# Optimization experiments

Hardware: AMD Instinct MI355X
Metric: run time of the kernel (lower is better)

Reference implementation:

```python
import jax, jax.numpy as jnp
import numpy as np

NEG_SLOPE = 0.2


def gat_layer(x, adj, W, a_src, a_dst):
    # x: (C, in_dim), adj: (C, C) 0/1, W: (in_dim, H*D), a_src/a_dst: (H, D)
    C = x.shape[0]
    H, D = a_src.shape
    h = (x @ W).reshape(C, H, D)            # (C, H, D)
    hh = jnp.transpose(h, (1, 0, 2))        # (H, C, D)
    asrc = jnp.einsum('hcd,hd->hc', hh, a_src)  # (H, C)
    adst = jnp.einsum('hcd,hd->hc', hh, a_dst)  # (H, C)
    e = asrc[:, :, None] + adst[:, None, :]     # (H, C, C)
    e = jax.nn.leaky_relu(e, NEG_SLOPE)
    e = jnp.where(adj[None, :, :] == 0, -jnp.inf, e)
    attn = jax.nn.softmax(e, axis=-1)           # (H, C, C)
    out = jnp.einsum('hij,hjd->hid', attn, hh)  # (H, C, D)
    return jnp.transpose(out, (1, 0, 2)).reshape(C, H * D)


def setup_inputs() -> dict:
    key = jax.random.key(0)
    ks = jax.random.split(key, 12)
    B, doc_dim = 1024, 768
    C, label_dim = 4096, 768
    hidden, H = 512, 4
    D = hidden // H  # 128

    doc_x = jax.random.normal(ks[0], (B, doc_dim), dtype=jnp.float32)
    label_init = jax.random.normal(ks[1], (C, label_dim), dtype=jnp.float32)
    adj = jax.random.randint(ks[2], (C, C), 0, 2, dtype=jnp.int32)
    adj = adj.at[jnp.arange(C), jnp.arange(C)].set(1)  # self-loops

    def xavier(k, shape):
        fan_in, fan_out = shape[0], shape[1]
        lim = jnp.sqrt(6.0 / (fan_in + fan_out)).astype(jnp.float32)
        return jax.random.uniform(k, shape, jnp.float32, -lim, lim)

    W1 = xavier(ks[3], (label_dim, hidden))
    a_src1 = xavier(ks[4], (H, D))
    a_dst1 = xavier(ks[5], (H, D))
    W2 = xavier(ks[6], (hidden, hidden))
    a_src2 = xavier(ks[7], (H, D))
    a_dst2 = xavier(ks[8], (H, D))
    Wd = xavier(ks[9], (doc_dim, hidden))
    bd = jnp.zeros((hidden,), jnp.float32)
    return {"doc_x": doc_x, "label_init": label_init, "adj": adj,
            "W1": W1, "a_src1": a_src1, "a_dst1": a_dst1,
            "W2": W2, "a_src2": a_src2, "a_dst2": a_dst2,
            "Wd": Wd, "bd": bd}


def reference(doc_x, label_init, adj, W1, a_src1, a_dst1, W2, a_src2, a_dst2, Wd, bd):
    # doc_proj (dropout = identity in eval)
    doc_h = jax.nn.relu(doc_x @ Wd + bd)            # (B, hidden)
    # label encoder: GAT -> ELU -> GAT
    h = gat_layer(label_init, adj, W1, a_src1, a_dst1)
    h = jax.nn.elu(h)
    label_h = gat_layer(h, adj, W2, a_src2, a_dst2)  # (C, hidden)
    logits = doc_h @ label_h.T                      # (B, C)
    return logits
```

## Files before the change

kernel.cpp:

```cpp
#include <hip/hip_runtime.h>
#include <hip/hip_bf16.h>
#include <math.h>

#define BDOCS   1024
#define CNODES  4096
#define INDIM   768
#define HID     512
#define NHEAD   4
#define HDIM    128
#define NEG_SLOPE 0.2f

#define KSPLIT  8
#define JPER    (CNODES / KSPLIT)
#define NCH     (JPER / 32)

typedef __attribute__((ext_vector_type(8))) short short8;
typedef __attribute__((ext_vector_type(4))) float f32x4;

__device__ __forceinline__ float lrelu(float x) { return x > 0.f ? x : NEG_SLOPE * x; }

__device__ __forceinline__ short f2bf(float f) {
    union { float f; unsigned u; } v; v.f = f;
    unsigned r = (v.u + 0x7fff + ((v.u >> 16) & 1)) >> 16;
    return (short)r;
}
__device__ __forceinline__ float bf2f(short s) {
    union { float f; unsigned u; } v; v.u = ((unsigned)(unsigned short)s) << 16;
    return v.f;
}
__device__ __forceinline__ unsigned pk2(float a, float b) {
    union { float f; unsigned u; } x, y; x.f = a; y.f = b;
    unsigned lo = (x.u + 0x7fff + ((x.u >> 16) & 1)) >> 16;
    unsigned hi = (y.u + 0x7fff + ((y.u >> 16) & 1)) >> 16;
    return lo | (hi << 16);
}
__device__ __forceinline__ short hup(float f) {
    union { float f; unsigned u; } v; v.f = f;
    return (short)((v.u + 0x8000) >> 16);
}

__device__ void frag_T_dev(const float* __restrict__ src, short* __restrict__ dst,
                           int N, int K, int jc, int nq, float (*tile)[132])
{
    const int t  = threadIdx.x;
    const int KC = K >> 5;
#pragma unroll
    for (int it = 0; it < 16; it++) {
        const int e = it * 256 + t;
        const int j = e >> 7, n = e & 127;
        tile[j][n] = src[(size_t)(jc * 32 + j) * N + nq * 128 + n];
    }
    __syncthreads();
#pragma unroll
    for (int s = 0; s < 2; s++) {
        const int item = s * 256 + t;
        const int nbl = item >> 6, lane = item & 63;
        const int nr = lane & 15, kq = lane >> 4;
        short8 v;
#pragma unroll
        for (int jr = 0; jr < 8; jr++)
            v[jr] = f2bf(tile[kq * 8 + jr][nbl * 16 + nr]);
        *(short8*)&dst[((size_t)((nq * 8 + nbl) * KC + jc) * 64 + lane) * 8] = v;
    }
}

__device__ void frag_A_dev(const float* __restrict__ src, short* __restrict__ dst,
                           int C, int rb, int cq, float (*tile)[132])
{
    const int t  = threadIdx.x;
    const int KC = C >> 5;
#pragma unroll
    for (int it = 0; it < 8; it++) {
        const int e = it * 256 + t;
        const int r = e >> 7, c = e & 127;
        tile[r][c] = src[(size_t)(rb * 16 + r) * C + cq * 128 + c];
    }
    __syncthreads();
    const int kcl = t >> 6, lane = t & 63;
    const int m = lane & 15, kq = lane >> 4;
    short8 v8;
#pragma unroll
    for (int j = 0; j < 8; j++) v8[j] = f2bf(tile[m][kcl * 32 + kq * 8 + j]);
    *(short8*)&dst[((size_t)(rb * KC + cq * 4 + kcl) * 64 + lane) * 8] = v8;
}

#define PREP_BLOCKS (65536 + 96 + 96 + 64 + 384 + 1536)
__global__ __launch_bounds__(256)
void prep_all(const int* __restrict__ adj, unsigned long long* __restrict__ adjb64,
              const float* __restrict__ Wd, short* __restrict__ Wdf,
              const float* __restrict__ W1, short* __restrict__ W1f,
              const float* __restrict__ W2, short* __restrict__ W2f,
              const float* __restrict__ doc_x, short* __restrict__ dxf,
              const float* __restrict__ label_init, short* __restrict__ lif)
{
    __shared__ float tile[32][132];
    int b = blockIdx.x;
    if (b < 65536) {
        const int t    = threadIdx.x;
        const int gw   = b * 4 + (t >> 6);
        const int lane = t & 63;
        const int i  = gw >> 6;
        const int j0 = (gw & 63) * 64;
        const int a  = adj[(size_t)i * CNODES + j0 + lane];
        const unsigned long long msk = __ballot(a != 0);
        if (lane == 0) adjb64[(size_t)i * 64 + (j0 >> 6)] = msk;
        return;
    }
    b -= 65536;
    if (b < 96)  { frag_T_dev(Wd, Wdf, HID, INDIM, b % 24, b / 24, tile); return; }
    b -= 96;
    if (b < 96)  { frag_T_dev(W1, W1f, HID, INDIM, b % 24, b / 24, tile); return; }
    b -= 96;
    if (b < 64)  { frag_T_dev(W2, W2f, HID, HID, b % 16, b / 16, tile); return; }
    b -= 64;
    if (b < 384) { frag_A_dev(doc_x, dxf, INDIM, b % 64, b / 64, tile); return; }
    b -= 384;
    frag_A_dev(label_init, lif, INDIM, b % 256, b / 256, tile);
}

template <int KC>
__global__ __launch_bounds__(64)
void gemm_hpre(const short* __restrict__ Af, const short* __restrict__ Bf,
               const float* __restrict__ a_src, const float* __restrict__ a_dst,
               short* __restrict__ hbTf, float* __restrict__ asrc, float* __restrict__ adst)
{
    __shared__ __align__(16) short tileT[128][24];
    const int lane = threadIdx.x;
    const int mb   = blockIdx.x;
    const int nq   = blockIdx.y;
    const int i0   = mb * 16;

    f32x4 acc[8];
#pragma unroll
    for (int c = 0; c < 8; c++) acc[c] = (f32x4){0.f, 0.f, 0.f, 0.f};

    const short* ap = Af + (size_t)mb * KC * 512 + lane * 8;
    const short* bp = Bf + (size_t)(nq * 8) * KC * 512 + lane * 8;

#pragma unroll 2
    for (int kc = 0; kc < KC; kc++) {
        short8 a = *(const short8*)(ap + (size_t)kc * 512);
#pragma unroll
        for (int c = 0; c < 8; c++) {
            short8 bf = *(const short8*)(bp + ((size_t)c * KC + kc) * 512);
            acc[c] = __builtin_amdgcn_mfma_f32_16x16x32_bf16(a, bf, acc[c], 0, 0, 0);
        }
    }

    const int col = lane & 15, q4 = lane >> 4;

#pragma unroll
    for (int c = 0; c < 8; c++) {
        uint2 u;
        u.x = pk2(acc[c][0], acc[c][1]);
        u.y = pk2(acc[c][2], acc[c][3]);
        *(uint2*)&tileT[c * 16 + col][q4 * 4] = u;
    }
    __syncthreads();
    {
        const int jc = mb >> 1, khalf = mb & 1;
        const int nr = lane & 15, kq = lane >> 4;
        if ((kq >> 1) == khalf) {
#pragma unroll
            for (int nbl = 0; nbl < 8; nbl++) {
                short8 v = *(const short8*)&tileT[nbl * 16 + nr][(kq & 1) * 8];
                *(short8*)&hbTf[(((size_t)(nq * 8 + nbl) * (CNODES / 32) + jc) * 64 + lane) * 8] = v;
            }
        }
    }

    float ssrc[4] = {}, sdst[4] = {};
#pragma unroll
    for (int c = 0; c < 8; c++) {
        const float vs = a_src[nq * 128 + c * 16 + col];
        const float vd = a_dst[nq * 128 + c * 16 + col];
#pragma unroll
        for (int r = 0; r < 4; r++) {
            ssrc[r] += acc[c][r] * vs;
            sdst[r] += acc[c][r] * vd;
        }
    }
#pragma unroll
    for (int mask = 1; mask <= 8; mask <<= 1)
#pragma unroll
        for (int r = 0; r < 4; r++) {
            ssrc[r] += __shfl_xor(ssrc[r], mask);
            sdst[r] += __shfl_xor(sdst[r], mask);
        }
    if (col == 0) {
#pragma unroll
        for (int r = 0; r < 4; r++) {
            const int row = i0 + q4 * 4 + r;
            asrc[nq * CNODES + row] = ssrc[r];
            adst[nq * CNODES + row] = sdst[r];
        }
    }
}

template <int KC>
__global__ __launch_bounds__(64)
void gemm_doc(const short* __restrict__ Af, const short* __restrict__ Bf,
              const float* __restrict__ bias, short* __restrict__ dhf)
{
    __shared__ __align__(16) short tile[16][64];
    const int lane = threadIdx.x;
    const int mb = blockIdx.x;
    const int ng = blockIdx.y;

    f32x4 acc[4];
#pragma unroll
    for (int c = 0; c < 4; c++) acc[c] = (f32x4){0.f, 0.f, 0.f, 0.f};

    const short* ap = Af + (size_t)mb * KC * 512 + lane * 8;
    const short* bp = Bf + (size_t)(ng * 4) * KC * 512 + lane * 8;

#pragma unroll 2
    for (int kc = 0; kc < KC; kc++) {
        short8 a = *(const short8*)(ap + (size_t)kc * 512);
#pragma unroll
        for (int c = 0; c < 4; c++) {
            short8 bf = *(const short8*)(bp + ((size_t)c * KC + kc) * 512);
            acc[c] = __builtin_amdgcn_mfma_f32_16x16x32_bf16(a, bf, acc[c], 0, 0, 0);
        }
    }

    const int col = lane & 15, q4 = lane >> 4;
#pragma unroll
    for (int c = 0; c < 4; c++)
#pragma unroll
        for (int r = 0; r < 4; r++) {
            float v = fmaxf(acc[c][r] + bias[ng * 64 + c * 16 + col], 0.f);
            tile[q4 * 4 + r][c * 16 + col] = f2bf(v);
        }
    __syncthreads();
    const int m = lane & 15, kq = lane >> 4;
#pragma unroll
    for (int kcl = 0; kcl < 2; kcl++) {
        short8 v = *(const short8*)&tile[m][kcl * 32 + kq * 8];
        *(short8*)&dhf[(((size_t)mb * 16 + ng * 2 + kcl) * 64 + lane) * 8] = v;
    }
}

template <int KC>
__global__ __launch_bounds__(64)
void gemm_frag(const short* __restrict__ Af, const short* __restrict__ Bf,
               float* __restrict__ Cmat, int N)
{
    const int lane = threadIdx.x;
    const int mb0  = blockIdx.x * 2;
    const int nq   = blockIdx.y;

    f32x4 acc[2][8];
#pragma unroll
    for (int f = 0; f < 2; f++)
#pragma unroll
        for (int c = 0; c < 8; c++) acc[f][c] = (f32x4){0.f, 0.f, 0.f, 0.f};

    const short* ap0 = Af + (size_t)mb0 * KC * 512 + lane * 8;
    const short* ap1 = ap0 + (size_t)KC * 512;
    const short* bp  = Bf + (size_t)(nq * 8) * KC * 512 + lane * 8;

#pragma unroll 2
    for (int kc = 0; kc < KC; kc++) {
        short8 a0 = *(const short8*)(ap0 + (size_t)kc * 512);
        short8 a1 = *(const short8*)(ap1 + (size_t)kc * 512);
#pragma unroll
        for (int c = 0; c < 8; c++) {
            short8 bf = *(const short8*)(bp + ((size_t)c * KC + kc) * 512);
            acc[0][c] = __builtin_amdgcn_mfma_f32_16x16x32_bf16(a0, bf, acc[0][c], 0, 0, 0);
            acc[1][c] = __builtin_amdgcn_mfma_f32_16x16x32_bf16(a1, bf, acc[1][c], 0, 0, 0);
        }
    }

    const int col = lane & 15, q4 = lane >> 4;
#pragma unroll
    for (int f = 0; f < 2; f++)
#pragma unroll
        for (int c = 0; c < 8; c++)
#pragma unroll
            for (int r = 0; r < 4; r++) {
                const int row = (mb0 + f) * 16 + q4 * 4 + r;
                Cmat[(size_t)row * N + nq * 128 + c * 16 + col] = acc[f][c][r];
            }
}

__global__ __launch_bounds__(1024)
void stats_exp(const float* __restrict__ adst, float* __restrict__ Mh,
               float* __restrict__ E1, float* __restrict__ E2)
{
    __shared__ float red[1024];
    __shared__ float s_mh;
    const int h = blockIdx.x, t = threadIdx.x;
    const float4 d4 = *(const float4*)(adst + (size_t)h * CNODES + t * 4);
    float m = fmaxf(fmaxf(d4.x, d4.y), fmaxf(d4.z, d4.w));
    red[t] = m; __syncthreads();
    for (int s = 512; s >= 1; s >>= 1) {
        if (t < s) red[t] = fmaxf(red[t], red[t + s]);
        __syncthreads();
    }
    if (t == 0) { s_mh = red[0]; Mh[h] = red[0]; }
    __syncthreads();
    const float mh = s_mh;
    float4 e1, e2;
    e1.x = __expf(d4.x - mh); e2.x = __expf(0.2f * (d4.x - mh));
    e1.y = __expf(d4.y - mh); e2.y = __expf(0.2f * (d4.y - mh));
    e1.z = __expf(d4.z - mh); e2.z = __expf(0.2f * (d4.z - mh));
    e1.w = __expf(d4.w - mh); e2.w = __expf(0.2f * (d4.w - mh));
    *(float4*)(E1 + (size_t)h * CNODES + t * 4) = e1;
    *(float4*)(E2 + (size_t)h * CNODES + t * 4) = e2;
}

__global__ __launch_bounds__(256, 2)
void attn_pv(const short* __restrict__ hbTf,
             const unsigned int* __restrict__ adjb,
             const float* __restrict__ asrc,
             const float* __restrict__ E1, const float* __restrict__ E2,
             const float* __restrict__ Mh,
             short* __restrict__ part, float* __restrict__ lpart)
{
    __shared__ __align__(16) short tileO[32][520];
    const int t    = threadIdx.x;
    const int w    = t >> 6;
    const int lane = t & 63;
    const int m    = lane & 15;
    const int kq   = lane >> 4;
    const int i0   = blockIdx.x * 64;
    const int ks   = blockIdx.y;
    const int js   = ks * JPER;

    const float mh = Mh[w];
    float A1[4], A2[4], T0[4];
#pragma unroll
    for (int g = 0; g < 4; g++) {
        const float as = asrc[w * CNODES + i0 + g * 16 + m];
        const float mr = lrelu(as + mh);
        A1[g] = __expf(as + mh - mr);
        A2[g] = __expf(0.2f * (as + mh) - mr);
        T0[g] = __expf(-as - mh);
    }

    f32x4 acc[4][8], accO[4];
#pragma unroll
    for (int g = 0; g < 4; g++) {
        accO[g] = (f32x4){0.f, 0.f, 0.f, 0.f};
#pragma unroll
        for (int c = 0; c < 8; c++) acc[g][c] = (f32x4){0.f, 0.f, 0.f, 0.f};
    }
    short8 ones;
#pragma unroll
    for (int q = 0; q < 8; q++) ones[q] = (short)0x3F80;

    for (int ch4 = 0; ch4 < 4; ch4++) {
        uint4 am[4];
#pragma unroll
        for (int g = 0; g < 4; g++)
            am[g] = *(const uint4*)(adjb + (size_t)(i0 + g * 16 + m) * 128 + ks * NCH + ch4 * 4);

#pragma unroll
        for (int chi = 0; chi < 4; chi++) {
            const int j0 = js + (ch4 * 4 + chi) * 32;
            unsigned aw[4];
#pragma unroll
            for (int g = 0; g < 4; g++)
                aw[g] = ((const unsigned*)&am[g])[chi] >> (kq * 8);

            const float4* p1 = (const float4*)(E1 + (size_t)w * CNODES + j0 + kq * 8);
            const float4* p2 = (const float4*)(E2 + (size_t)w * CNODES + j0 + kq * 8);
            const float4 x0 = p1[0], x1 = p1[1];
            const float4 y0 = p2[0], y1 = p2[1];
            const float e1v[8] = {x0.x, x0.y, x0.z, x0.w, x1.x, x1.y, x1.z, x1.w};
            const float e2v[8] = {y0.x, y0.y, y0.z, y0.w, y1.x, y1.y, y1.z, y1.w};

            short8 a[4];
#pragma unroll
            for (int q = 0; q < 8; q++) {
                const float e1 = e1v[q], e2 = e2v[q];
#pragma unroll
                for (int g = 0; g < 4; g++) {
                    const bool c0 = e1 > T0[g];
                    float wv = (c0 ? A1[g] : A2[g]) * (c0 ? e1 : e2);
                    wv = ((aw[g] >> q) & 1u) ? wv : 0.f;
                    a[g][q] = hup(wv);
                }
            }

            const short* bbase = hbTf + (((size_t)(w * 8) * 128 + (j0 >> 5)) * 64 + lane) * 8;
#pragma unroll
            for (int c = 0; c < 8; c++) {
                short8 bf = *(const short8*)(bbase + (size_t)c * 128 * 64 * 8);
                acc[0][c] = __builtin_amdgcn_mfma_f32_16x16x32_bf16(a[0], bf, acc[0][c], 0, 0, 0);
                acc[1][c] = __builtin_amdgcn_mfma_f32_16x16x32_bf16(a[1], bf, acc[1][c], 0, 0, 0);
                acc[2][c] = __builtin_amdgcn_mfma_f32_16x16x32_bf16(a[2], bf, acc[2][c], 0, 0, 0);
                acc[3][c] = __builtin_amdgcn_mfma_f32_16x16x32_bf16(a[3], bf, acc[3][c], 0, 0, 0);
            }
#pragma unroll
            for (int g = 0; g < 4; g++)
                accO[g] = __builtin_amdgcn_mfma_f32_16x16x32_bf16(a[g], ones, accO[g], 0, 0, 0);
        }
    }

    const int col = m, q4 = kq;
    if (m == 0) {
#pragma unroll
        for (int g = 0; g < 4; g++)
#pragma unroll
            for (int r = 0; r < 4; r++)
                lpart[((size_t)ks * NHEAD + w) * CNODES + i0 + g * 16 + q4 * 4 + r] = accO[g][r];
    }

    short* pS = part + (size_t)ks * CNODES * HID;
    for (int half = 0; half < 2; half++) {
        __syncthreads();
#pragma unroll
        for (int f = 0; f < 2; f++)
#pragma unroll
            for (int c = 0; c < 8; c++)
#pragma unroll
                for (int r = 0; r < 4; r++)
                    tileO[f * 16 + q4 * 4 + r][w * 128 + c * 16 + col] = f2bf(acc[half * 2 + f][c][r]);
        __syncthreads();
#pragma unroll
        for (int it = 0; it < 8; it++) {
            const int u   = it * 256 + t;
            const int row = u >> 6, un = u & 63;
            uint4 v = *(const uint4*)&tileO[row][un * 8];
            *(uint4*)&pS[(size_t)(i0 + half * 32 + row) * HID + un * 8] = v;
        }
    }
}

template <bool ELU>
__global__ __launch_bounds__(256)
void reduce_norm_frag(const short* __restrict__ part, const float* __restrict__ lpart,
                      short* __restrict__ dst)
{
    const int t = threadIdx.x;
    const int W = blockIdx.x * 4 + (t >> 6);
    const int lane = t & 63;
    const int rb = W >> 4, kc = W & 15;
    const int m = lane & 15, kq = lane >> 4;
    const int i = rb * 16 + m;
    const int n0 = kc * 32 + kq * 8;
    const int h = kc >> 2;

    float v[8] = {};
    float l = 0.f;
#pragma unroll
    for (int s = 0; s < KSPLIT; s++) {
        const uint4 raw = *(const uint4*)&part[(size_t)s * CNODES * HID + (size_t)i * HID + n0];
        const unsigned rr[4] = {raw.x, raw.y, raw.z, raw.w};
#pragma unroll
        for (int q = 0; q < 4; q++) {
            v[q * 2]     += bf2f((short)(rr[q] & 0xffff));
            v[q * 2 + 1] += bf2f((short)(rr[q] >> 16));
        }
        l += lpart[((size_t)s * NHEAD + h) * CNODES + i];
    }
    const float inv = 1.0f / l;
    short8 o;
#pragma unroll
    for (int q = 0; q < 8; q++) {
        float x = v[q] * inv;
        if (ELU) x = x > 0.f ? x : (__expf(x) - 1.f);
        o[q] = f2bf(x);
    }
    *(short8*)&dst[((size_t)(rb * 16 + kc) * 64 + lane) * 8] = o;
}

extern "C" void kernel_launch(void* const* d_in, const int* in_sizes, int n_in,
                              void* d_out, int out_size, void* d_ws, size_t ws_size,
                              hipStream_t stream)
{
    const float* doc_x      = (const float*)d_in[0];
    const float* label_init = (const float*)d_in[1];
    const int*   adj        = (const int*)d_in[2];
    const float* W1         = (const float*)d_in[3];
    const float* a_src1     = (const float*)d_in[4];
    const float* a_dst1     = (const float*)d_in[5];
    const float* W2         = (const float*)d_in[6];
    const float* a_src2     = (const float*)d_in[7];
    const float* a_dst2     = (const float*)d_in[8];
    const float* Wd         = (const float*)d_in[9];
    const float* bd         = (const float*)d_in[10];
    float*       out        = (float*)d_out;

    char* wsb = (char*)d_ws;
    size_t off = 0;
    auto alloc = [&](size_t bytes) -> char* {
        char* p = wsb + off;
        off = (off + bytes + 255) & ~(size_t)255;
        return p;
    };

    float* asrc  = (float*)alloc(NHEAD * CNODES * 4);
    float* adst  = (float*)alloc(NHEAD * CNODES * 4);
    float* Mh    = (float*)alloc(256);
    float* E1    = (float*)alloc(NHEAD * CNODES * 4);
    float* E2    = (float*)alloc(NHEAD * CNODES * 4);
    float* lpart = (float*)alloc((size_t)KSPLIT * NHEAD * CNODES * 4);
    unsigned int* adjb = (unsigned int*)alloc((size_t)CNODES * 128 * 4);
    short* hbTf  = (short*)alloc((size_t)CNODES * HID * 2);
    short* Wdf   = (short*)alloc((size_t)INDIM * HID * 2);
    short* W1f   = (short*)alloc((size_t)INDIM * HID * 2);
    short* W2f   = (short*)alloc((size_t)HID * HID * 2);
    short* dxf   = (short*)alloc((size_t)BDOCS * INDIM * 2);
    short* Af_li = (short*)alloc((size_t)CNODES * INDIM * 2);
    short* Af2   = (short*)alloc((size_t)CNODES * HID * 2);
    short* lhf   = (short*)alloc((size_t)CNODES * HID * 2);
    short* dhf   = (short*)alloc((size_t)BDOCS * HID * 2);
    short* part  = (short*)alloc((size_t)KSPLIT * CNODES * HID * 2);
    (void)ws_size;

    const dim3 blk(256);

    prep_all<<<PREP_BLOCKS, blk, 0, stream>>>(adj, (unsigned long long*)adjb,
                                              Wd, Wdf, W1, W1f, W2, W2f,
                                              doc_x, dxf, label_init, Af_li);

    gemm_doc<INDIM / 32><<<dim3(BDOCS / 16, HID / 64), 64, 0, stream>>>(dxf, Wdf, bd, dhf);

    gemm_hpre<INDIM / 32><<<dim3(CNODES / 16, NHEAD), 64, 0, stream>>>(
        Af_li, W1f, a_src1, a_dst1, hbTf, asrc, adst);

    stats_exp<<<NHEAD, 1024, 0, stream>>>(adst, Mh, E1, E2);
    attn_pv<<<dim3(CNODES / 64, KSPLIT), blk, 0, stream>>>(hbTf, adjb, asrc, E1, E2, Mh, part, lpart);
    reduce_norm_frag<true><<<CNODES * HID / 256 / 8, blk, 0, stream>>>(part, lpart, Af2);

    gemm_hpre<HID / 32><<<dim3(CNODES / 16, NHEAD), 64, 0, stream>>>(
        Af2, W2f, a_src2, a_dst2, hbTf, asrc, adst);

    stats_exp<<<NHEAD, 1024, 0, stream>>>(adst, Mh, E1, E2);
    attn_pv<<<dim3(CNODES / 64, KSPLIT), blk, 0, stream>>>(hbTf, adjb, asrc, E1, E2, Mh, part, lpart);
    reduce_norm_frag<false><<<CNODES * HID / 256 / 8, blk, 0, stream>>>(part, lpart, lhf);

    gemm_frag<HID / 32><<<dim3(BDOCS / 32, CNODES / 128), 64, 0, stream>>>(dhf, lhf, out, CNODES);
}
```

Measured before the change: 400.5 us.

## Fuse per-head max into GEMM via atomics and compute exp tables in attention LDS

Removes the separate stats_exp kernel. The per-head max of adst is now folded into gemm_hpre through an order-preserving float encoding and atomicMax, and each attn_pv block computes its own E1/E2 exp slices into shared memory. attn_pv is restructured to 512 threads, with each wave handling 32 rows instead of 64, which roughly halves per-thread accumulator registers and lets more waves run. In exchange, each column block recomputes its exp slice, atomics are added, and the encoded max buffer must be zeroed in prep_all.

```diff
diff --git a/kernel.cpp b/kernel.cpp
--- a/kernel.cpp
+++ b/kernel.cpp
@@ -38,6 +38,15 @@
     union { float f; unsigned u; } v; v.f = f;
     return (short)((v.u + 0x8000) >> 16);
 }
+__device__ __forceinline__ unsigned encf(float x) {
+    union { float f; unsigned u; } v; v.f = x;
+    return (v.u & 0x80000000u) ? ~v.u : (v.u | 0x80000000u);
+}
+__device__ __forceinline__ float decf(unsigned u) {
+    union { float f; unsigned u; } v;
+    v.u = (u & 0x80000000u) ? (u ^ 0x80000000u) : ~u;
+    return v.f;
+}
 
 __device__ void frag_T_dev(const float* __restrict__ src, short* __restrict__ dst,
                            int N, int K, int jc, int nq, float (*tile)[132])
@@ -91,11 +100,13 @@
               const float* __restrict__ W1, short* __restrict__ W1f,
               const float* __restrict__ W2, short* __restrict__ W2f,
               const float* __restrict__ doc_x, short* __restrict__ dxf,
-              const float* __restrict__ label_init, short* __restrict__ lif)
+              const float* __restrict__ label_init, short* __restrict__ lif,
+              unsigned* __restrict__ MhEnc)
 {
     __shared__ float tile[32][132];
     int b = blockIdx.x;
     if (b < 65536) {
+        if (b == 0 && threadIdx.x < 8) MhEnc[threadIdx.x] = 0u;
         const int t    = threadIdx.x;
         const int gw   = b * 4 + (t >> 6);
         const int lane = t & 63;
@@ -122,7 +133,8 @@
 __global__ __launch_bounds__(64)
 void gemm_hpre(const short* __restrict__ Af, const short* __restrict__ Bf,
                const float* __restrict__ a_src, const float* __restrict__ a_dst,
-               short* __restrict__ hbTf, float* __restrict__ asrc, float* __restrict__ adst)
+               short* __restrict__ hbTf, float* __restrict__ asrc, float* __restrict__ adst,
+               unsigned* __restrict__ MhEnc)
 {
     __shared__ __align__(16) short tileT[128][24];
     const int lane = threadIdx.x;
@@ -195,6 +207,10 @@
             adst[nq * CNODES + row] = sdst[r];
         }
     }
+    float wmax = fmaxf(fmaxf(sdst[0], sdst[1]), fmaxf(sdst[2], sdst[3]));
+    wmax = fmaxf(wmax, __shfl_xor(wmax, 16));
+    wmax = fmaxf(wmax, __shfl_xor(wmax, 32));
+    if (lane == 0) atomicMax(MhEnc + nq, encf(wmax));
 }
 
 template <int KC>
@@ -284,144 +300,123 @@
             }
 }
 
-__global__ __launch_bounds__(1024)
-void stats_exp(const float* __restrict__ adst, float* __restrict__ Mh,
-               float* __restrict__ E1, float* __restrict__ E2)
-{
-    __shared__ float red[1024];
-    __shared__ float s_mh;
-    const int h = blockIdx.x, t = threadIdx.x;
-    const float4 d4 = *(const float4*)(adst + (size_t)h * CNODES + t * 4);
-    float m = fmaxf(fmaxf(d4.x, d4.y), fmaxf(d4.z, d4.w));
-    red[t] = m; __syncthreads();
-    for (int s = 512; s >= 1; s >>= 1) {
-        if (t < s) red[t] = fmaxf(red[t], red[t + s]);
-        __syncthreads();
-    }
-    if (t == 0) { s_mh = red[0]; Mh[h] = red[0]; }
-    __syncthreads();
-    const float mh = s_mh;
-    float4 e1, e2;
-    e1.x = __expf(d4.x - mh); e2.x = __expf(0.2f * (d4.x - mh));
-    e1.y = __expf(d4.y - mh); e2.y = __expf(0.2f * (d4.y - mh));
-    e1.z = __expf(d4.z - mh); e2.z = __expf(0.2f * (d4.z - mh));
-    e1.w = __expf(d4.w - mh); e2.w = __expf(0.2f * (d4.w - mh));
-    *(float4*)(E1 + (size_t)h * CNODES + t * 4) = e1;
-    *(float4*)(E2 + (size_t)h * CNODES + t * 4) = e2;
-}
-
-__global__ __launch_bounds__(256, 2)
+__global__ __launch_bounds__(512, 2)
 void attn_pv(const short* __restrict__ hbTf,
              const unsigned int* __restrict__ adjb,
-             const float* __restrict__ asrc,
-             const float* __restrict__ E1, const float* __restrict__ E2,
-             const float* __restrict__ Mh,
+             const float* __restrict__ asrc, const float* __restrict__ adst,
+             const unsigned* __restrict__ MhEnc,
              short* __restrict__ part, float* __restrict__ lpart)
 {
+    __shared__ __align__(16) float E1s[NHEAD][512];
+    __shared__ __align__(16) float E2s[NHEAD][512];
     __shared__ __align__(16) short tileO[32][520];
+
     const int t    = threadIdx.x;
-    const int w    = t >> 6;
+    const int ww   = t >> 6;
+    const int w    = ww & 3;
+    const int f2   = ww >> 2;
     const int lane = t & 63;
     const int m    = lane & 15;
     const int kq   = lane >> 4;
     const int i0   = blockIdx.x * 64;
+    const int iw   = i0 + f2 * 32;
     const int ks   = blockIdx.y;
     const int js   = ks * JPER;
 
-    const float mh = Mh[w];
-    float A1[4], A2[4], T0[4];
-#pragma unroll
-    for (int g = 0; g < 4; g++) {
-        const float as = asrc[w * CNODES + i0 + g * 16 + m];
-        const float mr = lrelu(as + mh);
-        A1[g] = __expf(as + mh - mr);
-        A2[g] = __expf(0.2f * (as + mh) - mr);
-        T0[g] = __expf(-as - mh);
-    }
-
-    f32x4 acc[4][8], accO[4];
-#pragma unroll
-    for (int g = 0; g < 4; g++) {
-        accO[g] = (f32x4){0.f, 0.f, 0.f, 0.f};
-#pragma unroll
-        for (int c = 0; c < 8; c++) acc[g][c] = (f32x4){0.f, 0.f, 0.f, 0.f};
+    {
+        const int j = js + t;
+#pragma unroll
+        for (int h = 0; h < NHEAD; h++) {
+            const float d = adst[h * CNODES + j] - decf(MhEnc[h]);
+            E1s[h][t] = __expf(d);
+            E2s[h][t] = __expf(0.2f * d);
+        }
+    }
+
+    const float mh  = decf(MhEnc[w]);
+    const float as0 = asrc[w * CNODES + iw + m];
+    const float as1 = asrc[w * CNODES + iw + 16 + m];
+    const float mr0 = lrelu(as0 + mh), mr1 = lrelu(as1 + mh);
+    const float A10 = __expf(as0 + mh - mr0),          A11 = __expf(as1 + mh - mr1);
+    const float A20 = __expf(0.2f * (as0 + mh) - mr0), A21 = __expf(0.2f * (as1 + mh) - mr1);
+    const float T00 = __expf(-as0 - mh),               T01 = __expf(-as1 - mh);
+
+    f32x4 acc[2][8], accO[2];
+#pragma unroll
+    for (int f = 0; f < 2; f++) {
+        accO[f] = (f32x4){0.f, 0.f, 0.f, 0.f};
+#pragma unroll
+        for (int c = 0; c < 8; c++) acc[f][c] = (f32x4){0.f, 0.f, 0.f, 0.f};
     }
     short8 ones;
 #pragma unroll
     for (int q = 0; q < 8; q++) ones[q] = (short)0x3F80;
 
-    for (int ch4 = 0; ch4 < 4; ch4++) {
-        uint4 am[4];
-#pragma unroll
-        for (int g = 0; g < 4; g++)
-            am[g] = *(const uint4*)(adjb + (size_t)(i0 + g * 16 + m) * 128 + ks * NCH + ch4 * 4);
-
-#pragma unroll
-        for (int chi = 0; chi < 4; chi++) {
-            const int j0 = js + (ch4 * 4 + chi) * 32;
-            unsigned aw[4];
-#pragma unroll
-            for (int g = 0; g < 4; g++)
-                aw[g] = ((const unsigned*)&am[g])[chi] >> (kq * 8);
-
-            const float4* p1 = (const float4*)(E1 + (size_t)w * CNODES + j0 + kq * 8);
-            const float4* p2 = (const float4*)(E2 + (size_t)w * CNODES + j0 + kq * 8);
-            const float4 x0 = p1[0], x1 = p1[1];
-            const float4 y0 = p2[0], y1 = p2[1];
-            const float e1v[8] = {x0.x, x0.y, x0.z, x0.w, x1.x, x1.y, x1.z, x1.w};
-            const float e2v[8] = {y0.x, y0.y, y0.z, y0.w, y1.x, y1.y, y1.z, y1.w};
-
-            short8 a[4];
-#pragma unroll
-            for (int q = 0; q < 8; q++) {
-                const float e1 = e1v[q], e2 = e2v[q];
-#pragma unroll
-                for (int g = 0; g < 4; g++) {
-                    const bool c0 = e1 > T0[g];
-                    float wv = (c0 ? A1[g] : A2[g]) * (c0 ? e1 : e2);
-                    wv = ((aw[g] >> q) & 1u) ? wv : 0.f;
-                    a[g][q] = hup(wv);
-                }
-            }
-
-            const short* bbase = hbTf + (((size_t)(w * 8) * 128 + (j0 >> 5)) * 64 + lane) * 8;
-#pragma unroll
-            for (int c = 0; c < 8; c++) {
-                short8 bf = *(const short8*)(bbase + (size_t)c * 128 * 64 * 8);
-                acc[0][c] = __builtin_amdgcn_mfma_f32_16x16x32_bf16(a[0], bf, acc[0][c], 0, 0, 0);
-                acc[1][c] = __builtin_amdgcn_mfma_f32_16x16x32_bf16(a[1], bf, acc[1][c], 0, 0, 0);
-                acc[2][c] = __builtin_amdgcn_mfma_f32_16x16x32_bf16(a[2], bf, acc[2][c], 0, 0, 0);
-                acc[3][c] = __builtin_amdgcn_mfma_f32_16x16x32_bf16(a[3], bf, acc[3][c], 0, 0, 0);
-            }
-#pragma unroll
-            for (int g = 0; g < 4; g++)
-                accO[g] = __builtin_amdgcn_mfma_f32_16x16x32_bf16(a[g], ones, accO[g], 0, 0, 0);
-        }
-    }
-
-    const int col = m, q4 = kq;
+    const unsigned int* ar0 = adjb + (size_t)(iw + m) * 128 + ks * NCH;
+    const unsigned int* ar1 = adjb + (size_t)(iw + 16 + m) * 128 + ks * NCH;
+
+    __syncthreads();
+
+#pragma unroll 2
+    for (int ch = 0; ch < NCH; ch++) {
+        const int jl = ch * 32;
+        const unsigned int aw0 = ar0[ch] >> (kq * 8);
+        const unsigned int aw1 = ar1[ch] >> (kq * 8);
+        const float4 x0 = *(const float4*)&E1s[w][jl + kq * 8];
+        const float4 x1 = *(const float4*)&E1s[w][jl + kq * 8 + 4];
+        const float4 y0 = *(const float4*)&E2s[w][jl + kq * 8];
+        const float4 y1 = *(const float4*)&E2s[w][jl + kq * 8 + 4];
+        const float e1v[8] = {x0.x, x0.y, x0.z, x0.w, x1.x, x1.y, x1.z, x1.w};
+        const float e2v[8] = {y0.x, y0.y, y0.z, y0.w, y1.x, y1.y, y1.z, y1.w};
+
+        short8 a0, a1;
+#pragma unroll
+        for (int q = 0; q < 8; q++) {
+            const float e1 = e1v[q], e2 = e2v[q];
+            const bool c0 = e1 > T00, c1 = e1 > T01;
+            float w0 = (c0 ? A10 : A20) * (c0 ? e1 : e2);
+            float w1 = (c1 ? A11 : A21) * (c1 ? e1 : e2);
+            w0 = ((aw0 >> q) & 1u) ? w0 : 0.f;
+            w1 = ((aw1 >> q) & 1u) ? w1 : 0.f;
+            a0[q] = hup(w0);
+            a1[q] = hup(w1);
+        }
+
+        const short* bbase = hbTf + (((size_t)(w * 8) * 128 + ((js + jl) >> 5)) * 64 + lane) * 8;
+#pragma unroll
+        for (int c = 0; c < 8; c++) {
+            short8 bf = *(const short8*)(bbase + (size_t)c * 128 * 64 * 8);
+            acc[0][c] = __builtin_amdgcn_mfma_f32_16x16x32_bf16(a0, bf, acc[0][c], 0, 0, 0);
+            acc[1][c] = __builtin_amdgcn_mfma_f32_16x16x32_bf16(a1, bf, acc[1][c], 0, 0, 0);
+        }
+        accO[0] = __builtin_amdgcn_mfma_f32_16x16x32_bf16(a0, ones, accO[0], 0, 0, 0);
+        accO[1] = __builtin_amdgcn_mfma_f32_16x16x32_bf16(a1, ones, accO[1], 0, 0, 0);
+    }
+
     if (m == 0) {
 #pragma unroll
-        for (int g = 0; g < 4; g++)
+        for (int f = 0; f < 2; f++)
 #pragma unroll
             for (int r = 0; r < 4; r++)
-                lpart[((size_t)ks * NHEAD + w) * CNODES + i0 + g * 16 + q4 * 4 + r] = accO[g][r];
+                lpart[((size_t)ks * NHEAD + w) * CNODES + iw + f * 16 + kq * 4 + r] = accO[f][r];
     }
 
     short* pS = part + (size_t)ks * CNODES * HID;
     for (int half = 0; half < 2; half++) {
         __syncthreads();
-#pragma unroll
-        for (int f = 0; f < 2; f++)
-#pragma unroll
-            for (int c = 0; c < 8; c++)
-#pragma unroll
-                for (int r = 0; r < 4; r++)
-                    tileO[f * 16 + q4 * 4 + r][w * 128 + c * 16 + col] = f2bf(acc[half * 2 + f][c][r]);
+        if (f2 == half) {
+#pragma unroll
+            for (int f = 0; f < 2; f++)
+#pragma unroll
+                for (int c = 0; c < 8; c++)
+#pragma unroll
+                    for (int r = 0; r < 4; r++)
+                        tileO[f * 16 + kq * 4 + r][w * 128 + c * 16 + m] = f2bf(acc[f][c][r]);
+        }
         __syncthreads();
 #pragma unroll
-        for (int it = 0; it < 8; it++) {
-            const int u   = it * 256 + t;
+        for (int it = 0; it < 4; it++) {
+            const int u   = it * 512 + t;
             const int row = u >> 6, un = u & 63;
             uint4 v = *(const uint4*)&tileO[row][un * 8];
             *(uint4*)&pS[(size_t)(i0 + half * 32 + row) * HID + un * 8] = v;
@@ -494,9 +489,7 @@
 
     float* asrc  = (float*)alloc(NHEAD * CNODES * 4);
     float* adst  = (float*)alloc(NHEAD * CNODES * 4);
-    float* Mh    = (float*)alloc(256);
-    float* E1    = (float*)alloc(NHEAD * CNODES * 4);
-    float* E2    = (float*)alloc(NHEAD * CNODES * 4);
+    unsigned* MhEnc = (unsigned*)alloc(256);
     float* lpart = (float*)alloc((size_t)KSPLIT * NHEAD * CNODES * 4);
     unsigned int* adjb = (unsigned int*)alloc((size_t)CNODES * 128 * 4);
     short* hbTf  = (short*)alloc((size_t)CNODES * HID * 2);
@@ -515,22 +508,22 @@
 
     prep_all<<<PREP_BLOCKS, blk, 0, stream>>>(adj, (unsigned long long*)adjb,
                                               Wd, Wdf, W1, W1f, W2, W2f,
-                                              doc_x, dxf, label_init, Af_li);
+                                              doc_x, dxf, label_init, Af_li, MhEnc);
 
     gemm_doc<INDIM / 32><<<dim3(BDOCS / 16, HID / 64), 64, 0, stream>>>(dxf, Wdf, bd, dhf);
 
     gemm_hpre<INDIM / 32><<<dim3(CNODES / 16, NHEAD), 64, 0, stream>>>(
-        Af_li, W1f, a_src1, a_dst1, hbTf, asrc, adst);
-
-    stats_exp<<<NHEAD, 1024, 0, stream>>>(adst, Mh, E1, E2);
-    attn_pv<<<dim3(CNODES / 64, KSPLIT), blk, 0, stream>>>(hbTf, adjb, asrc, E1, E2, Mh, part, lpart);
+        Af_li, W1f, a_src1, a_dst1, hbTf, asrc, adst, MhEnc);
+
+    attn_pv<<<dim3(CNODES / 64, KSPLIT), 512, 0, stream>>>(
+        hbTf, adjb, asrc, adst, MhEnc, part, lpart);
     reduce_norm_frag<true><<<CNODES * HID / 256 / 8, blk, 0, stream>>>(part, lpart, Af2);
 
     gemm_hpre<HID / 32><<<dim3(CNODES / 16, NHEAD), 64, 0, stream>>>(
-        Af2, W2f, a_src2, a_dst2, hbTf, asrc, adst);
-
-    stats_exp<<<NHEAD, 1024, 0, stream>>>(adst, Mh, E1, E2);
-    attn_pv<<<dim3(CNODES / 64, KSPLIT), blk, 0, stream>>>(hbTf, adjb, asrc, E1, E2, Mh, part, lpart);
+        Af2, W2f, a_src2, a_dst2, hbTf, asrc, adst, MhEnc + 4);
+
+    attn_pv<<<dim3(CNODES / 64, KSPLIT), 512, 0, stream>>>(
+        hbTf, adjb, asrc, adst, MhEnc + 4, part, lpart);
     reduce_norm_frag<false><<<CNODES * HID / 256 / 8, blk, 0, stream>>>(part, lpart, lhf);
 
     gemm_frag<HID / 32><<<dim3(BDOCS / 32, CNODES / 128), 64, 0, stream>>>(dhf, lhf, out, CNODES);
```

After: 394.1 us. No clear change (-1.6%).
